# Kernel optimization log

Measured on AMD Instinct MI355X. Metric: run time of the kernel, lower is better.

## Reference

```python
import jax, jax.numpy as jnp
import numpy as np

ZERO = 1e-8
L = 2            # num_gnn_layers
D = 256          # dim_node_features
B = 32           # graphs per batch
NPG = 256        # nodes per graph
N = B * NPG      # total nodes
E = 131072       # edges per edge-type
MAX_TOKENS = 256 # MAX_TOKENS_OF_A_POST
UPD = 0.5        # args.updated_weights_for_A


def _make_edges(k):
    k1, k2, k3 = jax.random.split(k, 3)
    g = jax.random.randint(k1, (E,), 0, B) * NPG          # keep edges within a graph
    src = g + jax.random.randint(k2, (E,), 0, NPG)
    dst = g + jax.random.randint(k3, (E,), 0, NPG)
    return jnp.stack([src, dst]).astype(jnp.int64)


def setup_inputs() -> dict:
    key = jax.random.key(0)
    ks = jax.random.split(key, 12)
    x = jax.random.normal(ks[0], (N, D), dtype=jnp.float32)
    ei_e = _make_edges(ks[1]); ew_e = jax.random.uniform(ks[2], (E,), dtype=jnp.float32)
    ei_p = _make_edges(ks[3]); ew_p = jax.random.uniform(ks[4], (E,), dtype=jnp.float32)
    ei_o = _make_edges(ks[5]); ew_o = jax.random.uniform(ks[6], (E,), dtype=jnp.float32)
    entity_mask = jax.random.randint(ks[7], (B, NPG), 0, 2).astype(bool)
    pattern_mask = jax.random.randint(ks[8], (B, NPG), 0, 2).astype(bool)
    s = 1.0 / np.sqrt(D)
    W_gcn = (jax.random.normal(ks[9], (L, 3, D, D), dtype=jnp.float32) * s)
    b_gcn = jnp.zeros((L, 3, D), dtype=jnp.float32)
    T_dyn = (jax.random.normal(ks[10], (L, D, D), dtype=jnp.float32) * s)
    return {
        'x': x,
        'edge_index_entity': ei_e, 'edge_weight_entity': ew_e,
        'edge_index_pattern': ei_p, 'edge_weight_pattern': ew_p,
        'edge_index_others': ei_o, 'edge_weight_others': ew_o,
        'entity_mask': entity_mask, 'pattern_mask': pattern_mask,
        'W_gcn': W_gcn, 'b_gcn': b_gcn, 'T_dyn': T_dyn,
    }


def _normalized_correlation_matrix(H):
    # cosine-similarity correlation matrix, symmetrically degree-normalized
    nrm = jnp.sqrt(jnp.sum(H * H, axis=1))
    A = (H @ H.T) / (nrm[:, None] * nrm[None, :] + ZERO)
    dinv = 1.0 / jnp.sqrt(jnp.abs(jnp.sum(A, axis=1)) + ZERO)
    return dinv[:, None] * A * dinv[None, :]


def _gcn(H, W, b, ei, ew):
    # GCNConv(add_self_loops=False, normalize=False): scatter-sum of weighted source messages
    msg = (H @ W)[ei[0]] * ew[:, None]                     # [E, D]
    return jax.ops.segment_sum(msg, ei[1], num_segments=N) + b


def _forward(x, we0, wp0, wo0, W_gcn, b_gcn, T_dyn,
             ei_e, ei_p, ei_o, entity_mask, pattern_mask):
    H = x
    A = _normalized_correlation_matrix(H)                  # [N, N]
    for i in range(L):
        if i == 0:
            we, wp, wo = we0, wp0, wo0
        else:
            # diag(one_hot(src) @ A @ one_hot(dst).T) == A[src, dst]
            we = A[ei_e[0], ei_e[1]]
            wp = A[ei_p[0], ei_p[1]]
            wo = A[ei_o[0], ei_o[1]]
        He = _gcn(H, W_gcn[i, 0], b_gcn[i, 0], ei_e, we)
        Hp = _gcn(H, W_gcn[i, 1], b_gcn[i, 1], ei_p, wp)
        Ho = _gcn(H, W_gcn[i, 2], b_gcn[i, 2], ei_o, wo)
        H = jax.nn.relu(He + Hp + Ho)
        A_hat = jax.nn.sigmoid((H @ T_dyn[i]) @ H.T)
        A = (1.0 - UPD) * A + UPD * A_hat
    # per-graph diagonal blocks of A  -> [B, NPG, NPG]
    A4 = A.reshape(B, NPG, B, NPG)
    idx = jnp.arange(B)
    blocks = A4[idx, :, idx, :]
    A_sum = jnp.sum(blocks, axis=-1)                       # [B, NPG]
    ent_cols = jnp.einsum('bij,bj->bi', blocks, entity_mask.astype(A.dtype))
    pat_cols = jnp.einsum('bij,bj->bi', blocks, pattern_mask.astype(A.dtype))
    map_pattern = A_sum - ent_cols
    map_entity = A_sum - pat_cols

    def finish(m):
        mn = jnp.min(m, axis=1, keepdims=True)
        mx = jnp.max(m, axis=1, keepdims=True)
        m = (m - mn) / (mx - mn + ZERO)
        m = m / (jnp.sum(m, axis=1, keepdims=True) + ZERO)
        return m[:, :MAX_TOKENS]                           # padding() with NPG==MAX_TOKENS

    return finish(map_entity), finish(map_pattern)


def reference(x, edge_index_entity, edge_weight_entity,
              edge_index_pattern, edge_weight_pattern,
              edge_index_others, edge_weight_others,
              entity_mask, pattern_mask, W_gcn, b_gcn, T_dyn):
    return _forward(x, edge_weight_entity, edge_weight_pattern, edge_weight_others,
                    W_gcn, b_gcn, T_dyn,
                    edge_index_entity, edge_index_pattern, edge_index_others,
                    entity_mask, pattern_mask)
```

## Files before the change

kernel.cpp:

```cpp
#include <hip/hip_runtime.h>

#define NND   8192
#define DDIM  256
#define NGRP  32
#define ZEROF 1e-8f
#define LSTR  40
#define TSTR  72
#define OFF_AH 0
#define OFF_AL 2560
#define OFF_BH 5120
#define OFF_BL 10240
#define OFF_TT 5120
#define LDS_U16 15360

typedef unsigned short u16;
typedef __attribute__((ext_vector_type(8))) short short8v;
typedef __attribute__((ext_vector_type(4))) float float4v;

__device__ inline u16 f2bf(float x) {
  unsigned u = __float_as_uint(x);
  u += 0x7fffu + ((u >> 16) & 1u);
  return (u16)(u >> 16);
}
__device__ inline float bf2f(u16 h) { return __uint_as_float((unsigned)h << 16); }
__device__ inline void split2(float x, u16& h, u16& l) {
  h = f2bf(x);
  l = f2bf(x - bf2f(h));
}

__device__ inline float wave_sum(float v) {
#pragma unroll
  for (int off = 32; off > 0; off >>= 1) v += __shfl_down(v, off, 64);
  return v;
}

#define LOAD_REGS(tt, kk)                                                                   \
  {                                                                                         \
    int m_ = tid >> 2, kq_ = (tid & 3) * 8;                                                 \
    size_t aoff_;                                                                           \
    if (MODE == 1)                                                                          \
      aoff_ = (size_t)((tt) * 256 + bym * 64 + m_) * 8192 + (size_t)(g * 256 + (kk) + kq_); \
    else if (MODE == 2 || MODE == 3)                                                        \
      aoff_ = (size_t)(g * 256 + bym * 64 + m_) * 256 + (kk) + kq_;                         \
    else                                                                                    \
      aoff_ = (size_t)(bym * 64 + m_) * 256 + (kk) + kq_;                                   \
    rAh = *(const short8v*)&Ah_g[aoff_];                                                    \
    rAl = *(const short8v*)&Al_g[aoff_];                                                    \
    if (MODE == 1) {                                                                        \
      int n_ = tid >> 2, kq2_ = (tid & 3) * 8;                                              \
      const float* pb_ = Bfp + (((size_t)g * 3 + (tt)) << 16) +                             \
                         (size_t)(col0 + n_) * 256 + (kk) + kq2_;                           \
      rBf[0] = *(const float4*)pb_;                                                         \
      rBf[1] = *(const float4*)(pb_ + 4);                                                   \
    } else if (HALF) {                                                                      \
      int n_ = tid & 63, kq2_ = (tid >> 6) * 8;                                             \
      size_t boff_ = (size_t)(((MODE == 2 || MODE == 3) ? g * 256 : 0) + col0 + n_) * 256   \
                     + (kk) + kq2_;                                                         \
      rBh0 = *(const short8v*)&Bh_g[boff_];                                                 \
      rBl0 = *(const short8v*)&Bl_g[boff_];                                                 \
    } else {                                                                                \
      int n_ = tid & 127, kq2_ = (tid >> 7) * 16;                                           \
      size_t boff_ = (size_t)(col0 + n_) * 256 + (kk) + kq2_;                               \
      rBh0 = *(const short8v*)&Bh_g[boff_]; rBh1 = *(const short8v*)&Bh_g[boff_ + 8];       \
      rBl0 = *(const short8v*)&Bl_g[boff_]; rBl1 = *(const short8v*)&Bl_g[boff_ + 8];       \
    }                                                                                       \
  }

template<int MODE, bool HALF>
__device__ __forceinline__ void mfma_body(
    u16* lds,
    const u16* __restrict__ Ah_g, const u16* __restrict__ Al_g,
    const u16* __restrict__ Bh_g, const u16* __restrict__ Bl_g,
    const float* __restrict__ Bfp,
    float* __restrict__ Cf, u16* __restrict__ Ch, u16* __restrict__ Cl,
    const float* __restrict__ nrm, const float* __restrict__ dinv,
    const float* __restrict__ bias,
    int bxm, int bym, int g) {
  u16* Ahs = lds + OFF_AH;
  u16* Als = lds + OFF_AL;
  u16* Bhs = lds + OFF_BH;
  u16* Bls = lds + OFF_BL;
  u16* Tt  = lds + OFF_TT;
  const int NJ = HALF ? 2 : 4;
  const int tid = threadIdx.x;
  const int col0 = bxm * (HALF ? 64 : 128);
  const int w = tid >> 6, lane = tid & 63;
  const int lm = lane & 15, lq = lane >> 4;
  const int wr = (w >> 1) * 32, wc = (w & 1) * (HALF ? 32 : 64);

  float4v acc[2][4];
#pragma unroll
  for (int i = 0; i < 2; ++i)
#pragma unroll
    for (int j = 0; j < NJ; ++j) acc[i][j] = (float4v)0.f;

  short8v rAh, rAl, rBh0, rBh1, rBl0, rBl1;
  float4 rBf[2];
  const int TOTAL = (MODE == 1) ? 24 : 8;

  LOAD_REGS(0, 0);
  for (int step = 0; step < TOTAL; ++step) {
    if (step) __syncthreads();
    {
      int m = tid >> 2, kq = (tid & 3) * 8;
      *(short8v*)&Ahs[m * LSTR + kq] = rAh;
      *(short8v*)&Als[m * LSTR + kq] = rAl;
    }
    if (MODE == 1) {
      int n = tid >> 2, kq2 = (tid & 3) * 8;
      u16 hh[8], ll[8];
      split2(rBf[0].x, hh[0], ll[0]); split2(rBf[0].y, hh[1], ll[1]);
      split2(rBf[0].z, hh[2], ll[2]); split2(rBf[0].w, hh[3], ll[3]);
      split2(rBf[1].x, hh[4], ll[4]); split2(rBf[1].y, hh[5], ll[5]);
      split2(rBf[1].z, hh[6], ll[6]); split2(rBf[1].w, hh[7], ll[7]);
      *(short8v*)&Bhs[n * LSTR + kq2] = *(short8v*)hh;
      *(short8v*)&Bls[n * LSTR + kq2] = *(short8v*)ll;
    } else if (HALF) {
      int n = tid & 63, kq2 = (tid >> 6) * 8;
      *(short8v*)&Bhs[n * LSTR + kq2] = rBh0;
      *(short8v*)&Bls[n * LSTR + kq2] = rBl0;
    } else {
      int n = tid & 127, kq2 = (tid >> 7) * 16;
      *(short8v*)&Bhs[n * LSTR + kq2] = rBh0; *(short8v*)&Bhs[n * LSTR + kq2 + 8] = rBh1;
      *(short8v*)&Bls[n * LSTR + kq2] = rBl0; *(short8v*)&Bls[n * LSTR + kq2 + 8] = rBl1;
    }
    __syncthreads();
    int nxt = step + 1;
    if (nxt < TOTAL) {
      int tt = nxt >> 3, kk = (nxt & 7) * 32;
      LOAD_REGS(tt, kk);
    }
    short8v ah[2], al[2], bh[4], bl[4];
#pragma unroll
    for (int i = 0; i < 2; ++i) {
      int r = wr + i * 16 + lm;
      ah[i] = *(const short8v*)&Ahs[r * LSTR + lq * 8];
      al[i] = *(const short8v*)&Als[r * LSTR + lq * 8];
    }
#pragma unroll
    for (int j = 0; j < NJ; ++j) {
      int r = wc + j * 16 + lm;
      bh[j] = *(const short8v*)&Bhs[r * LSTR + lq * 8];
      bl[j] = *(const short8v*)&Bls[r * LSTR + lq * 8];
    }
#pragma unroll
    for (int i = 0; i < 2; ++i)
#pragma unroll
      for (int j = 0; j < NJ; ++j) {
        acc[i][j] = __builtin_amdgcn_mfma_f32_16x16x32_bf16(ah[i], bh[j], acc[i][j], 0, 0, 0);
        acc[i][j] = __builtin_amdgcn_mfma_f32_16x16x32_bf16(ah[i], bl[j], acc[i][j], 0, 0, 0);
        acc[i][j] = __builtin_amdgcn_mfma_f32_16x16x32_bf16(al[i], bh[j], acc[i][j], 0, 0, 0);
      }
  }

  if (MODE == 2 || MODE == 3) {
#pragma unroll
    for (int i = 0; i < 2; ++i) {
#pragma unroll
      for (int r = 0; r < 4; ++r) {
        int grow = g * 256 + bym * 64 + wr + i * 16 + lq * 4 + r;
        float di = 0.f, ni = 0.f;
        if (MODE == 2) { di = dinv[grow]; ni = nrm[grow]; }
#pragma unroll
        for (int j = 0; j < NJ; ++j) {
          int gcol = col0 + wc + j * 16 + lm;
          size_t ci = (size_t)grow * 256 + gcol;
          float v = acc[i][j][r];
          if (MODE == 2) {
            int gj = g * 256 + gcol;
            Cf[ci] = v * di * dinv[gj] / (ni * nrm[gj] + ZEROF);
          } else {
            Cf[ci] = 0.5f * Cf[ci] + 0.5f * (1.f / (1.f + expf(-v)));
          }
        }
      }
    }
  } else {
    float bsum[8];
    if (MODE == 1) {
#pragma unroll
      for (int i = 0; i < 2; ++i)
#pragma unroll
        for (int r = 0; r < 4; ++r) {
          int d = bym * 64 + wr + i * 16 + lq * 4 + r;
          bsum[i * 4 + r] = bias[d] + bias[256 + d] + bias[512 + d];
        }
    }
    u16 hv[32], lv[32];
#pragma unroll
    for (int i = 0; i < 2; ++i)
#pragma unroll
      for (int j = 0; j < NJ; ++j)
#pragma unroll
        for (int r = 0; r < 4; ++r) {
          float v = acc[i][j][r];
          if (MODE == 1) v = fmaxf(v + bsum[i * 4 + r], 0.f);
          split2(v, hv[(i * 4 + r) * NJ + j], lv[(i * 4 + r) * NJ + j]);
        }
    int ebase1 = (MODE == 1) ? (g * 256 + col0) : col0;
    int ebase2 = bym * 64;
    size_t estride = (MODE == 0) ? 8192 : 256;
#pragma unroll
    for (int ph = 0; ph < 2; ++ph) {
      __syncthreads();
      const u16* sv = ph ? lv : hv;
#pragma unroll
      for (int i = 0; i < 2; ++i)
#pragma unroll
        for (int j = 0; j < NJ; ++j)
#pragma unroll
          for (int r = 0; r < 4; ++r)
            Tt[(wc + j * 16 + lm) * TSTR + wr + i * 16 + lq * 4 + r] = sv[(i * 4 + r) * NJ + j];
      __syncthreads();
      u16* dst = ph ? Cl : Ch;
      int cc0 = tid >> 3, mm0 = (tid & 7) * 8;
#pragma unroll
      for (int it = 0; it < (HALF ? 2 : 4); ++it) {
        int cc = it * 32 + cc0;
        short8v v = *(const short8v*)&Tt[cc * TSTR + mm0];
        *(short8v*)&dst[(size_t)(ebase1 + cc) * estride + ebase2 + mm0] = v;
      }
    }
  }
}

__global__ void k_prep(const int* __restrict__ e0, const int* __restrict__ e1,
                       const int* __restrict__ e2, const unsigned char* __restrict__ m0,
                       const unsigned char* __restrict__ m1,
                       const float* __restrict__ W, const float* __restrict__ T,
                       const float* __restrict__ x,
                       int* __restrict__ eo, float* __restrict__ emf, float* __restrict__ pmf,
                       u16* __restrict__ Wth, u16* __restrict__ Wtl,
                       float* __restrict__ Mzero,
                       float* __restrict__ nrm, float* __restrict__ Spart,
                       u16* __restrict__ Hh, u16* __restrict__ Hl,
                       int E2, int nCvt) {
  __shared__ float tile[32][33];
  __shared__ float inv[64];
  __shared__ int nz[2];
  const int b = blockIdx.x, tid = threadIdx.x;
  if (b < nCvt) {
    if (tid < 2) nz[tid] = 0;
    __syncthreads();
    if (e0[2 * tid + 1] != 0) atomicAdd(&nz[0], 1);
    int i4 = tid * 4;
    int c = (m0[i4 + 1] != 0) + (m0[i4 + 2] != 0) + (m0[i4 + 3] != 0);
    if (c) atomicAdd(&nz[1], c);
    __syncthreads();
    int fE = (nz[0] == 0), fM = (nz[1] == 0);
    int i = b * 256 + tid;
    if (i < E2) {
      eo[i] = fE ? e0[2 * i] : e0[i];
    } else if (i < 2 * E2) {
      int j = i - E2; eo[E2 + j] = fE ? e1[2 * j] : e1[j];
    } else if (i < 3 * E2) {
      int j = i - 2 * E2; eo[2 * E2 + j] = fE ? e2[2 * j] : e2[j];
    } else if (i < 3 * E2 + NND) {
      int j = i - 3 * E2; unsigned char v = fM ? m0[4 * j] : m0[j];
      emf[j] = 1.f - (float)(v != 0);
    } else if (i < 3 * E2 + 2 * NND) {
      int j = i - 3 * E2 - NND; unsigned char v = fM ? m1[4 * j] : m1[j];
      pmf[j] = 1.f - (float)(v != 0);
    }
  } else if (b < nCvt + 512) {
    int bb = b - nCvt;
    int mat = bb >> 6, rem = bb & 63;
    int k0 = (rem >> 3) * 32, n0 = (rem & 7) * 32;
    const float* src = (mat < 6) ? (W + (size_t)mat * 65536) : (T + (size_t)(mat - 6) * 65536);
    int r = tid >> 3, c4 = (tid & 7) * 4;
    const float4 v = *(const float4*)&src[(size_t)(k0 + r) * 256 + n0 + c4];
    tile[r][c4 + 0] = v.x; tile[r][c4 + 1] = v.y; tile[r][c4 + 2] = v.z; tile[r][c4 + 3] = v.w;
    __syncthreads();
    float o[4] = {tile[c4 + 0][r], tile[c4 + 1][r], tile[c4 + 2][r], tile[c4 + 3][r]};
    u16 hh[4], ll[4];
#pragma unroll
    for (int q = 0; q < 4; ++q) split2(o[q], hh[q], ll[q]);
    size_t off = (size_t)mat * 65536 + (size_t)(n0 + r) * 256 + k0 + c4;
    *(ushort4*)&Wth[off] = *(ushort4*)hh;
    *(ushort4*)&Wtl[off] = *(ushort4*)ll;
  } else if (b < nCvt + 512 + 3072) {
    int bb = b - nCvt - 512;
    float4* p = (float4*)Mzero;
    size_t base = (size_t)bb * 1024 + tid;
    float4 z = make_float4(0.f, 0.f, 0.f, 0.f);
    p[base] = z; p[base + 256] = z; p[base + 512] = z; p[base + 768] = z;
  } else {
    int bn = b - nCvt - 512 - 3072;
    int n0 = bn * 64;
    int w = tid >> 6, lane = tid & 63;
    for (int it = 0; it < 16; ++it) {
      int nl = it * 4 + w;
      int node = n0 + nl;
      const float4 v = *(const float4*)&x[(size_t)node * 256 + lane * 4];
      u16 hh[4], ll[4];
      split2(v.x, hh[0], ll[0]); split2(v.y, hh[1], ll[1]);
      split2(v.z, hh[2], ll[2]); split2(v.w, hh[3], ll[3]);
      *(ushort4*)&Hh[(size_t)node * 256 + lane * 4] = *(ushort4*)hh;
      *(ushort4*)&Hl[(size_t)node * 256 + lane * 4] = *(ushort4*)ll;
      float s = wave_sum(v.x * v.x + v.y * v.y + v.z * v.z + v.w * v.w);
      if (lane == 0) { float nr = sqrtf(s); nrm[node] = nr; inv[nl] = 1.f / nr; }
    }
    __syncthreads();
    float s = 0.f;
    for (int i = 0; i < 64; ++i) s += x[(size_t)(n0 + i) * 256 + tid] * inv[i];
    Spart[bn * 256 + tid] = s;
  }
}

__global__ __launch_bounds__(256, 2) void k_stageA(
    const u16* __restrict__ Hinh, const u16* __restrict__ Hinl,
    const u16* __restrict__ Wth, const u16* __restrict__ Wtl, int l,
    u16* __restrict__ XWTh, u16* __restrict__ XWTl,
    const int* __restrict__ edges, const float* __restrict__ ew0,
    const float* __restrict__ ew1, const float* __restrict__ ew2,
    const float* __restrict__ Abuf, float* __restrict__ Mb, int E_,
    const float* __restrict__ x, const float* __restrict__ Spart,
    const float* __restrict__ nrm, float* __restrict__ dinv) {
  __shared__ u16 lds[LDS_U16];
  const int b = blockIdx.x;
  if (b < 768) {
    mfma_body<0, false>(lds, Hinh, Hinl, Wth + (size_t)l * 768 * 256,
                        Wtl + (size_t)l * 768 * 256, nullptr,
                        nullptr, XWTh, XWTl, nullptr, nullptr, nullptr,
                        b >> 7, b & 127, 0);
  } else if (b < 1024) {
    int bi = b - 768;
    for (int i = bi * 256 + threadIdx.x; i < 3 * E_; i += 65536) {
      int t = i / E_;
      int e = i - t * E_;
      const int* ei = edges + (size_t)t * 2 * E_;
      int src = ei[e], dst = ei[E_ + e];
      float wgt = l ? Abuf[(size_t)src * 256 + (dst & 255)]
                    : (t == 0 ? ew0 : (t == 1 ? ew1 : ew2))[e];
      int gg = src >> 8;
      atomicAdd(&Mb[(((size_t)gg * 3 + t) << 16) + ((size_t)(dst & 255) << 8) + (src & 255)],
                wgt);
    }
  } else {
    float* Sl = (float*)lds;
    const int tid = threadIdx.x;
    float s = 0.f;
    for (int bb = 0; bb < 128; ++bb) s += Spart[bb * 256 + tid];
    Sl[tid] = s;
    __syncthreads();
    int base = (b - 1024) * 64;
    int w = tid >> 6, lane = tid & 63;
    const float4 sv = *(const float4*)&Sl[lane * 4];
    for (int it = 0; it < 16; ++it) {
      int node = base + it * 4 + w;
      const float4 v = *(const float4*)&x[(size_t)node * 256 + lane * 4];
      float s2 = wave_sum(v.x * sv.x + v.y * sv.y + v.z * sv.z + v.w * sv.w);
      if (lane == 0) {
        float rowsum = s2 / nrm[node];
        dinv[node] = rsqrtf(fabsf(rowsum) + ZEROF);
      }
    }
  }
}

__global__ __launch_bounds__(256, 2) void k_stageB(
    const u16* __restrict__ XWTh, const u16* __restrict__ XWTl,
    const float* __restrict__ Mb,
    u16* __restrict__ Houth, u16* __restrict__ Houtl, const float* __restrict__ bias,
    const u16* __restrict__ xh, const u16* __restrict__ xl, float* __restrict__ Abuf,
    const float* __restrict__ nrm, const float* __restrict__ dinv) {
  __shared__ u16 lds[LDS_U16];
  const int b = blockIdx.x;
  if (b < 512) {
    int g = b & 31, r = b >> 5;
    mfma_body<1, true>(lds, XWTh, XWTl, nullptr, nullptr, Mb,
                       nullptr, Houth, Houtl, nullptr, nullptr, bias,
                       r >> 2, r & 3, g);
  } else {
    int bb = b - 512;
    int g = bb & 31, r = bb >> 5;
    mfma_body<2, true>(lds, xh, xl, xh, xl, nullptr, Abuf, nullptr, nullptr,
                       nrm, dinv, nullptr, r >> 2, r & 3, g);
  }
}

__global__ __launch_bounds__(256, 2) void k_stageC(
    const u16* __restrict__ Wth, const u16* __restrict__ Wtl, int l,
    const u16* __restrict__ Hh, const u16* __restrict__ Hl,
    u16* __restrict__ tmph, u16* __restrict__ tmpl) {
  __shared__ u16 lds[LDS_U16];
  const int b = blockIdx.x;
  mfma_body<4, true>(lds, Wth + (size_t)(6 + l) * 65536, Wtl + (size_t)(6 + l) * 65536,
                     Hh, Hl, nullptr, nullptr, tmph, tmpl, nullptr, nullptr, nullptr,
                     b & 127, b >> 7, 0);
}

__global__ __launch_bounds__(256, 2) void k_stageD(
    const u16* __restrict__ tmph, const u16* __restrict__ tmpl,
    const u16* __restrict__ Hh, const u16* __restrict__ Hl,
    float* __restrict__ Abuf) {
  __shared__ u16 lds[LDS_U16];
  const int b = blockIdx.x;
  int g = b & 31, r = b >> 5;
  mfma_body<3, true>(lds, tmph, tmpl, Hh, Hl, nullptr, Abuf, nullptr, nullptr,
                     nullptr, nullptr, nullptr, r >> 2, r & 3, g);
}

__global__ void k_maps(const float* __restrict__ Abuf, const float* __restrict__ emf,
                       const float* __restrict__ pmf, float* __restrict__ out) {
  __shared__ float sme[256], smp[256], red[256];
  const int g = blockIdx.x, tid = threadIdx.x, w = tid >> 6, lane = tid & 63;
  const int j0 = g * 256 + lane * 4;
  const float4 pmv = *(const float4*)&pmf[j0];
  const float4 emv = *(const float4*)&emf[j0];
  for (int it = 0; it < 64; ++it) {
    int nl = it * 4 + w;
    const float4 a = *(const float4*)&Abuf[((size_t)g * 256 + nl) * 256 + lane * 4];
    float me = a.x * pmv.x + a.y * pmv.y + a.z * pmv.z + a.w * pmv.w;
    float mp = a.x * emv.x + a.y * emv.y + a.z * emv.z + a.w * emv.w;
#pragma unroll
    for (int off = 32; off > 0; off >>= 1) {
      me += __shfl_down(me, off, 64);
      mp += __shfl_down(mp, off, 64);
    }
    if (lane == 0) { sme[nl] = me; smp[nl] = mp; }
  }
  __syncthreads();
  for (int which = 0; which < 2; ++which) {
    float v = which ? smp[tid] : sme[tid];
    red[tid] = v; __syncthreads();
    for (int s = 128; s > 0; s >>= 1) { if (tid < s) red[tid] = fminf(red[tid], red[tid + s]); __syncthreads(); }
    float mn = red[0]; __syncthreads();
    red[tid] = v; __syncthreads();
    for (int s = 128; s > 0; s >>= 1) { if (tid < s) red[tid] = fmaxf(red[tid], red[tid + s]); __syncthreads(); }
    float mx = red[0]; __syncthreads();
    float m = (v - mn) / (mx - mn + ZEROF);
    red[tid] = m; __syncthreads();
    for (int s = 128; s > 0; s >>= 1) { if (tid < s) red[tid] += red[tid + s]; __syncthreads(); }
    float sum = red[0]; __syncthreads();
    out[which * NND + g * 256 + tid] = m / (sum + ZEROF);
  }
}

extern "C" void kernel_launch(void* const* d_in, const int* in_sizes, int n_in,
                              void* d_out, int out_size, void* d_ws, size_t ws_size,
                              hipStream_t stream) {
  const float* x = (const float*)d_in[0];
  const unsigned char* em_raw = (const unsigned char*)d_in[7];
  const unsigned char* pm_raw = (const unsigned char*)d_in[8];
  const float* W  = (const float*)d_in[9];
  const float* bg = (const float*)d_in[10];
  const float* T  = (const float*)d_in[11];
  float* out = (float*)d_out;
  const int E_ = in_sizes[2];
  const int E2 = 2 * E_;

  float* ws = (float*)d_ws;
  size_t o = 0;
  float* Abuf = ws + o; o += (size_t)NND * 256;
  float* Mb3  = ws + o; o += (size_t)2 * NGRP * 3 * 65536;
  u16* Hh   = (u16*)(ws + o); o += (size_t)NND * 256 / 2;
  u16* Hl   = (u16*)(ws + o); o += (size_t)NND * 256 / 2;
  u16* H2h  = (u16*)(ws + o); o += (size_t)NND * 256 / 2;
  u16* H2l  = (u16*)(ws + o); o += (size_t)NND * 256 / 2;
  u16* tmph = (u16*)(ws + o); o += (size_t)NND * 256 / 2;
  u16* tmpl = (u16*)(ws + o); o += (size_t)NND * 256 / 2;
  u16* XWTh = (u16*)(ws + o); o += (size_t)768 * NND / 2;
  u16* XWTl = (u16*)(ws + o); o += (size_t)768 * NND / 2;
  u16* Wth  = (u16*)(ws + o); o += (size_t)8 * 65536 / 2;
  u16* Wtl  = (u16*)(ws + o); o += (size_t)8 * 65536 / 2;
  float* nrm   = ws + o; o += NND;
  float* dinv  = ws + o; o += NND;
  float* Spart = ws + o; o += 128 * 256;
  float* emf   = ws + o; o += NND;
  float* pmf   = ws + o; o += NND;
  int* edges   = (int*)(ws + o); o += (size_t)3 * E2;

  const float* ew0 = (const float*)d_in[2];
  const float* ew1 = (const float*)d_in[4];
  const float* ew2 = (const float*)d_in[6];
  float* Mb_l0 = Mb3;
  float* Mb_l1 = Mb3 + (size_t)NGRP * 3 * 65536;

  const int nCvt = (3 * E2 + 2 * NND + 255) / 256;

  k_prep<<<nCvt + 512 + 3072 + 128, 256, 0, stream>>>(
      (const int*)d_in[1], (const int*)d_in[3], (const int*)d_in[5], em_raw, pm_raw,
      W, T, x, edges, emf, pmf, Wth, Wtl, Mb3, nrm, Spart, Hh, Hl, E2, nCvt);

  k_stageA<<<1152, 256, 0, stream>>>(Hh, Hl, Wth, Wtl, 0, XWTh, XWTl,
                                     edges, ew0, ew1, ew2, Abuf, Mb_l0, E_,
                                     x, Spart, nrm, dinv);
  k_stageB<<<1024, 256, 0, stream>>>(XWTh, XWTl, Mb_l0, H2h, H2l, bg,
                                     Hh, Hl, Abuf, nrm, dinv);
  k_stageC<<<512, 256, 0, stream>>>(Wth, Wtl, 0, H2h, H2l, tmph, tmpl);
  k_stageD<<<512, 256, 0, stream>>>(tmph, tmpl, H2h, H2l, Abuf);

  k_stageA<<<1024, 256, 0, stream>>>(H2h, H2l, Wth, Wtl, 1, XWTh, XWTl,
                                     edges, ew0, ew1, ew2, Abuf, Mb_l1, E_,
                                     x, Spart, nrm, dinv);
  k_stageB<<<512, 256, 0, stream>>>(XWTh, XWTl, Mb_l1, Hh, Hl, bg + 768,
                                    nullptr, nullptr, nullptr, nullptr, nullptr);
  k_stageC<<<512, 256, 0, stream>>>(Wth, Wtl, 1, Hh, Hl, tmph, tmpl);
  k_stageD<<<512, 256, 0, stream>>>(tmph, tmpl, Hh, Hl, Abuf);

  k_maps<<<NGRP, 256, 0, stream>>>(Abuf, emf, pmf, out);
}
```

Before: 287.9 us.

## Build layer-1 adjacency from edge counts inside stageD epilogue, remove second scatter pass

Layer 0 now scatters both the edge weight and an edge count into an interleaved buffer. The layer-1 dense adjacency is built in the stageD epilogue by multiplying the counts by the freshly computed correlation values, which replaces the second atomic scatter over all edges. The layer-1 X@W GEMM also merges into the same launch as the layer-0 T GEMM, removing one launch. The cost is double the atomics in layer 0, strided float loads in stageB0, and an extra dense write of the per-graph blocks in stageD. This assumes edge weights in layer 1 depend only on the (src, dst) pair.

Result: slower. 342.6 us (+19.0%).

```diff
diff --git a/kernel.cpp b/kernel.cpp
--- a/kernel.cpp
+++ b/kernel.cpp
@@ -48,10 +48,15 @@
     rAl = *(const short8v*)&Al_g[aoff_];                                                    \
     if (MODE == 1) {                                                                        \
       int n_ = tid >> 2, kq2_ = (tid & 3) * 8;                                              \
-      const float* pb_ = Bfp + (((size_t)g * 3 + (tt)) << 16) +                             \
-                         (size_t)(col0 + n_) * 256 + (kk) + kq2_;                           \
-      rBf[0] = *(const float4*)pb_;                                                         \
-      rBf[1] = *(const float4*)(pb_ + 4);                                                   \
+      size_t cb_ = (((size_t)g * 3 + (tt)) << 16) + (size_t)(col0 + n_) * 256 + (kk) + kq2_;\
+      if (STRIDED) {                                                                        \
+        const float* pb_ = Bfp + cb_ * 2;                                                   \
+        rBf[0] = *(const float4*)pb_;        rBf[1] = *(const float4*)(pb_ + 4);            \
+        rBf[2] = *(const float4*)(pb_ + 8);  rBf[3] = *(const float4*)(pb_ + 12);           \
+      } else {                                                                              \
+        const float* pb_ = Bfp + cb_;                                                       \
+        rBf[0] = *(const float4*)pb_;        rBf[1] = *(const float4*)(pb_ + 4);            \
+      }                                                                                     \
     } else if (HALF) {                                                                      \
       int n_ = tid & 63, kq2_ = (tid >> 6) * 8;                                             \
       size_t boff_ = (size_t)(((MODE == 2 || MODE == 3) ? g * 256 : 0) + col0 + n_) * 256   \
@@ -66,7 +71,7 @@
     }                                                                                       \
   }
 
-template<int MODE, bool HALF>
+template<int MODE, bool HALF, bool STRIDED = false>
 __device__ __forceinline__ void mfma_body(
     u16* lds,
     const u16* __restrict__ Ah_g, const u16* __restrict__ Al_g,
@@ -95,7 +100,7 @@
     for (int j = 0; j < NJ; ++j) acc[i][j] = (float4v)0.f;
 
   short8v rAh, rAl, rBh0, rBh1, rBl0, rBl1;
-  float4 rBf[2];
+  float4 rBf[4];
   const int TOTAL = (MODE == 1) ? 24 : 8;
 
   LOAD_REGS(0, 0);
@@ -108,11 +113,17 @@
     }
     if (MODE == 1) {
       int n = tid >> 2, kq2 = (tid & 3) * 8;
+      float vals[8];
+      if (STRIDED) {
+        vals[0] = rBf[0].x; vals[1] = rBf[0].z; vals[2] = rBf[1].x; vals[3] = rBf[1].z;
+        vals[4] = rBf[2].x; vals[5] = rBf[2].z; vals[6] = rBf[3].x; vals[7] = rBf[3].z;
+      } else {
+        vals[0] = rBf[0].x; vals[1] = rBf[0].y; vals[2] = rBf[0].z; vals[3] = rBf[0].w;
+        vals[4] = rBf[1].x; vals[5] = rBf[1].y; vals[6] = rBf[1].z; vals[7] = rBf[1].w;
+      }
       u16 hh[8], ll[8];
-      split2(rBf[0].x, hh[0], ll[0]); split2(rBf[0].y, hh[1], ll[1]);
-      split2(rBf[0].z, hh[2], ll[2]); split2(rBf[0].w, hh[3], ll[3]);
-      split2(rBf[1].x, hh[4], ll[4]); split2(rBf[1].y, hh[5], ll[5]);
-      split2(rBf[1].z, hh[6], ll[6]); split2(rBf[1].w, hh[7], ll[7]);
+#pragma unroll
+      for (int q = 0; q < 8; ++q) split2(vals[q], hh[q], ll[q]);
       *(short8v*)&Bhs[n * LSTR + kq2] = *(short8v*)hh;
       *(short8v*)&Bls[n * LSTR + kq2] = *(short8v*)ll;
     } else if (HALF) {
@@ -154,6 +165,7 @@
   }
 
   if (MODE == 2 || MODE == 3) {
+    float anewv[2][2][4];
 #pragma unroll
     for (int i = 0; i < 2; ++i) {
 #pragma unroll
@@ -170,8 +182,40 @@
             int gj = g * 256 + gcol;
             Cf[ci] = v * di * dinv[gj] / (ni * nrm[gj] + ZEROF);
           } else {
-            Cf[ci] = 0.5f * Cf[ci] + 0.5f * (1.f / (1.f + expf(-v)));
+            float nv = 0.5f * Cf[ci] + 0.5f * (1.f / (1.f + expf(-v)));
+            Cf[ci] = nv;
+            anewv[i][j][r] = nv;
           }
+        }
+      }
+    }
+    if (MODE == 3 && Ch != nullptr) {
+      const float* MCb = Bfp;
+      float* M1 = (float*)Ch;
+      float* Af = (float*)lds;
+      __syncthreads();
+#pragma unroll
+      for (int i = 0; i < 2; ++i)
+#pragma unroll
+        for (int j = 0; j < 2; ++j)
+#pragma unroll
+          for (int r = 0; r < 4; ++r)
+            Af[(wc + j * 16 + lm) * 65 + (wr + i * 16 + lq * 4 + r)] = anewv[i][j][r];
+      __syncthreads();
+      int rr = tid >> 2;
+      int q4 = (tid & 3) * 16;
+#pragma unroll
+      for (int t = 0; t < 3; ++t) {
+        size_t cb = (((size_t)g * 3 + t) << 16) + (size_t)(col0 + rr) * 256 + bym * 64 + q4;
+#pragma unroll
+        for (int v = 0; v < 4; ++v) {
+          const float4 p0 = *(const float4*)&MCb[(cb + v * 4) * 2];
+          const float4 p1 = *(const float4*)&MCb[(cb + v * 4) * 2 + 4];
+          float a0 = Af[rr * 65 + q4 + v * 4 + 0];
+          float a1 = Af[rr * 65 + q4 + v * 4 + 1];
+          float a2 = Af[rr * 65 + q4 + v * 4 + 2];
+          float a3 = Af[rr * 65 + q4 + v * 4 + 3];
+          *(float4*)&M1[cb + v * 4] = make_float4(p0.y * a0, p0.w * a1, p1.y * a2, p1.w * a3);
         }
       }
     }
@@ -231,7 +275,7 @@
                        const float* __restrict__ x,
                        int* __restrict__ eo, float* __restrict__ emf, float* __restrict__ pmf,
                        u16* __restrict__ Wth, u16* __restrict__ Wtl,
-                       float* __restrict__ Mzero,
+                       float* __restrict__ MCzero,
                        float* __restrict__ nrm, float* __restrict__ Spart,
                        u16* __restrict__ Hh, u16* __restrict__ Hl,
                        int E2, int nCvt) {
@@ -280,7 +324,7 @@
     *(ushort4*)&Wtl[off] = *(ushort4*)ll;
   } else if (b < nCvt + 512 + 3072) {
     int bb = b - nCvt - 512;
-    float4* p = (float4*)Mzero;
+    float4* p = (float4*)MCzero;
     size_t base = (size_t)bb * 1024 + tid;
     float4 z = make_float4(0.f, 0.f, 0.f, 0.f);
     p[base] = z; p[base + 256] = z; p[base + 512] = z; p[base + 768] = z;
@@ -309,18 +353,17 @@
 
 __global__ __launch_bounds__(256, 2) void k_stageA(
     const u16* __restrict__ Hinh, const u16* __restrict__ Hinl,
-    const u16* __restrict__ Wth, const u16* __restrict__ Wtl, int l,
+    const u16* __restrict__ Wth, const u16* __restrict__ Wtl,
     u16* __restrict__ XWTh, u16* __restrict__ XWTl,
     const int* __restrict__ edges, const float* __restrict__ ew0,
     const float* __restrict__ ew1, const float* __restrict__ ew2,
-    const float* __restrict__ Abuf, float* __restrict__ Mb, int E_,
+    float* __restrict__ MC, int E_,
     const float* __restrict__ x, const float* __restrict__ Spart,
     const float* __restrict__ nrm, float* __restrict__ dinv) {
   __shared__ u16 lds[LDS_U16];
   const int b = blockIdx.x;
   if (b < 768) {
-    mfma_body<0, false>(lds, Hinh, Hinl, Wth + (size_t)l * 768 * 256,
-                        Wtl + (size_t)l * 768 * 256, nullptr,
+    mfma_body<0, false>(lds, Hinh, Hinl, Wth, Wtl, nullptr,
                         nullptr, XWTh, XWTl, nullptr, nullptr, nullptr,
                         b >> 7, b & 127, 0);
   } else if (b < 1024) {
@@ -330,11 +373,11 @@
       int e = i - t * E_;
       const int* ei = edges + (size_t)t * 2 * E_;
       int src = ei[e], dst = ei[E_ + e];
-      float wgt = l ? Abuf[(size_t)src * 256 + (dst & 255)]
-                    : (t == 0 ? ew0 : (t == 1 ? ew1 : ew2))[e];
+      float wgt = (t == 0 ? ew0 : (t == 1 ? ew1 : ew2))[e];
       int gg = src >> 8;
-      atomicAdd(&Mb[(((size_t)gg * 3 + t) << 16) + ((size_t)(dst & 255) << 8) + (src & 255)],
-                wgt);
+      size_t idx = (((size_t)gg * 3 + t) << 16) + ((size_t)(dst & 255) << 8) + (src & 255);
+      atomicAdd(&MC[idx * 2], wgt);
+      atomicAdd(&MC[idx * 2 + 1], 1.f);
     }
   } else {
     float* Sl = (float*)lds;
@@ -358,9 +401,9 @@
   }
 }
 
-__global__ __launch_bounds__(256, 2) void k_stageB(
+__global__ __launch_bounds__(256, 2) void k_stageB0(
     const u16* __restrict__ XWTh, const u16* __restrict__ XWTl,
-    const float* __restrict__ Mb,
+    const float* __restrict__ MC,
     u16* __restrict__ Houth, u16* __restrict__ Houtl, const float* __restrict__ bias,
     const u16* __restrict__ xh, const u16* __restrict__ xl, float* __restrict__ Abuf,
     const float* __restrict__ nrm, const float* __restrict__ dinv) {
@@ -368,9 +411,9 @@
   const int b = blockIdx.x;
   if (b < 512) {
     int g = b & 31, r = b >> 5;
-    mfma_body<1, true>(lds, XWTh, XWTl, nullptr, nullptr, Mb,
-                       nullptr, Houth, Houtl, nullptr, nullptr, bias,
-                       r >> 2, r & 3, g);
+    mfma_body<1, true, true>(lds, XWTh, XWTl, nullptr, nullptr, MC,
+                             nullptr, Houth, Houtl, nullptr, nullptr, bias,
+                             r >> 2, r & 3, g);
   } else {
     int bb = b - 512;
     int g = bb & 31, r = bb >> 5;
@@ -379,13 +422,44 @@
   }
 }
 
-__global__ __launch_bounds__(256, 2) void k_stageC(
-    const u16* __restrict__ Wth, const u16* __restrict__ Wtl, int l,
+__global__ __launch_bounds__(256, 2) void k_stageB1(
+    const u16* __restrict__ XWTh, const u16* __restrict__ XWTl,
+    const float* __restrict__ Mb,
+    u16* __restrict__ Houth, u16* __restrict__ Houtl, const float* __restrict__ bias) {
+  __shared__ u16 lds[LDS_U16];
+  const int b = blockIdx.x;
+  int g = b & 31, r = b >> 5;
+  mfma_body<1, true, false>(lds, XWTh, XWTl, nullptr, nullptr, Mb,
+                            nullptr, Houth, Houtl, nullptr, nullptr, bias,
+                            r >> 2, r & 3, g);
+}
+
+__global__ __launch_bounds__(256, 2) void k_stageCA(
+    const u16* __restrict__ Wth, const u16* __restrict__ Wtl,
+    const u16* __restrict__ H2h, const u16* __restrict__ H2l,
+    u16* __restrict__ tmph, u16* __restrict__ tmpl,
+    u16* __restrict__ XWTh, u16* __restrict__ XWTl) {
+  __shared__ u16 lds[LDS_U16];
+  const int b = blockIdx.x;
+  if (b < 512) {
+    mfma_body<4, true>(lds, Wth + (size_t)6 * 65536, Wtl + (size_t)6 * 65536,
+                       H2h, H2l, nullptr, nullptr, tmph, tmpl, nullptr, nullptr, nullptr,
+                       b & 127, b >> 7, 0);
+  } else {
+    int bb = b - 512;
+    mfma_body<0, false>(lds, H2h, H2l, Wth + (size_t)768 * 256, Wtl + (size_t)768 * 256,
+                        nullptr, nullptr, XWTh, XWTl, nullptr, nullptr, nullptr,
+                        bb >> 7, bb & 127, 0);
+  }
+}
+
+__global__ __launch_bounds__(256, 2) void k_stageC1(
+    const u16* __restrict__ Wth, const u16* __restrict__ Wtl,
     const u16* __restrict__ Hh, const u16* __restrict__ Hl,
     u16* __restrict__ tmph, u16* __restrict__ tmpl) {
   __shared__ u16 lds[LDS_U16];
   const int b = blockIdx.x;
-  mfma_body<4, true>(lds, Wth + (size_t)(6 + l) * 65536, Wtl + (size_t)(6 + l) * 65536,
+  mfma_body<4, true>(lds, Wth + (size_t)7 * 65536, Wtl + (size_t)7 * 65536,
                      Hh, Hl, nullptr, nullptr, tmph, tmpl, nullptr, nullptr, nullptr,
                      b & 127, b >> 7, 0);
 }
@@ -393,11 +467,11 @@
 __global__ __launch_bounds__(256, 2) void k_stageD(
     const u16* __restrict__ tmph, const u16* __restrict__ tmpl,
     const u16* __restrict__ Hh, const u16* __restrict__ Hl,
-    float* __restrict__ Abuf) {
+    float* __restrict__ Abuf, const float* __restrict__ MC, float* __restrict__ M1) {
   __shared__ u16 lds[LDS_U16];
   const int b = blockIdx.x;
   int g = b & 31, r = b >> 5;
-  mfma_body<3, true>(lds, tmph, tmpl, Hh, Hl, nullptr, Abuf, nullptr, nullptr,
+  mfma_body<3, true>(lds, tmph, tmpl, Hh, Hl, MC, Abuf, (u16*)M1, nullptr,
                      nullptr, nullptr, nullptr, r >> 2, r & 3, g);
 }
 
@@ -453,7 +527,8 @@
   float* ws = (float*)d_ws;
   size_t o = 0;
   float* Abuf = ws + o; o += (size_t)NND * 256;
-  float* Mb3  = ws + o; o += (size_t)2 * NGRP * 3 * 65536;
+  float* MC   = ws + o; o += (size_t)2 * NGRP * 3 * 65536;
+  float* Mb1  = ws + o; o += (size_t)NGRP * 3 * 65536;
   u16* Hh   = (u16*)(ws + o); o += (size_t)NND * 256 / 2;
   u16* Hl   = (u16*)(ws + o); o += (size_t)NND * 256 / 2;
   u16* H2h  = (u16*)(ws + o); o += (size_t)NND * 256 / 2;
@@ -474,30 +549,24 @@
   const float* ew0 = (const float*)d_in[2];
   const float* ew1 = (const float*)d_in[4];
   const float* ew2 = (const float*)d_in[6];
-  float* Mb_l0 = Mb3;
-  float* Mb_l1 = Mb3 + (size_t)NGRP * 3 * 65536;
 
   const int nCvt = (3 * E2 + 2 * NND + 255) / 256;
 
   k_prep<<<nCvt + 512 + 3072 + 128, 256, 0, stream>>>(
       (const int*)d_in[1], (const int*)d_in[3], (const int*)d_in[5], em_raw, pm_raw,
-      W, T, x, edges, emf, pmf, Wth, Wtl, Mb3, nrm, Spart, Hh, Hl, E2, nCvt);
-
-  k_stageA<<<1152, 256, 0, stream>>>(Hh, Hl, Wth, Wtl, 0, XWTh, XWTl,
-                                     edges, ew0, ew1, ew2, Abuf, Mb_l0, E_,
+      W, T, x, edges, emf, pmf, Wth, Wtl, MC, nrm, Spart, Hh, Hl, E2, nCvt);
+
+  k_stageA<<<1152, 256, 0, stream>>>(Hh, Hl, Wth, Wtl, XWTh, XWTl,
+                                     edges, ew0, ew1, ew2, MC, E_,
                                      x, Spart, nrm, dinv);
-  k_stageB<<<1024, 256, 0, stream>>>(XWTh, XWTl, Mb_l0, H2h, H2l, bg,
-                                     Hh, Hl, Abuf, nrm, dinv);
-  k_stageC<<<512, 256, 0, stream>>>(Wth, Wtl, 0, H2h, H2l, tmph, tmpl);
-  k_stageD<<<512, 256, 0, stream>>>(tmph, tmpl, H2h, H2l, Abuf);
-
-  k_stageA<<<1024, 256, 0, stream>>>(H2h, H2l, Wth, Wtl, 1, XWTh, XWTl,
-                                     edges, ew0, ew1, ew2, Abuf, Mb_l1, E_,
-                                     x, Spart, nrm, dinv);
-  k_stageB<<<512, 256, 0, stream>>>(XWTh, XWTl, Mb_l1, Hh, Hl, bg + 768,
-                                    nullptr, nullptr, nullptr, nullptr, nullptr);
-  k_stageC<<<512, 256, 0, stream>>>(Wth, Wtl, 1, Hh, Hl, tmph, tmpl);
-  k_stageD<<<512, 256, 0, stream>>>(tmph, tmpl, Hh, Hl, Abuf);
+  k_stageB0<<<1024, 256, 0, stream>>>(XWTh, XWTl, MC, H2h, H2l, bg,
+                                      Hh, Hl, Abuf, nrm, dinv);
+  k_stageCA<<<1280, 256, 0, stream>>>(Wth, Wtl, H2h, H2l, tmph, tmpl, XWTh, XWTl);
+  k_stageD<<<512, 256, 0, stream>>>(tmph, tmpl, H2h, H2l, Abuf, MC, Mb1);
+
+  k_stageB1<<<512, 256, 0, stream>>>(XWTh, XWTl, Mb1, Hh, Hl, bg + 768);
+  k_stageC1<<<512, 256, 0, stream>>>(Wth, Wtl, Hh, Hl, tmph, tmpl);
+  k_stageD<<<512, 256, 0, stream>>>(tmph, tmpl, Hh, Hl, Abuf, nullptr, nullptr);
 
   k_maps<<<NGRP, 256, 0, stream>>>(Abuf, emf, pmf, out);
 }
```
